# Performance work log

Measured on AMD Instinct MI355X. Metric: run time of the kernel, lower is better.

## Reference

```python
import jax, jax.numpy as jnp
import numpy as np
from jax import lax
from jax.scipy.special import logsumexp

TEMP_MIN, TEMP_MAX = 0.1, 1.0
B, I, J, C = 2, 128, 512, 256


def setup_inputs() -> dict:
    key = jax.random.key(0)
    k1, k2, k3 = jax.random.split(key, 3)
    return {
        "text_embeddings": jax.random.normal(k1, (B, I, C), dtype=jnp.float32),
        "mel_embeddings": jax.random.normal(k2, (B, J, C), dtype=jnp.float32),
        "text_mask": jnp.ones((B, I), dtype=jnp.float32),
        "mel_mask": jnp.ones((B, J), dtype=jnp.float32),
        "noise": jax.random.gumbel(k3, (B, I, J), dtype=jnp.float32),  # -log(-log(U))
        "temperature_ratio": jnp.float32(0.5),
    }


def _cond_prob(energy, text_mask, mel_mask, direction):
    # energy: [B, I, J]; returns [B, I, J, K] log conditional probs (normalized over axis 2)
    b, i, j = energy.shape
    if direction == "alpha":
        k = j
        tri = jnp.arange(j)[:, None] >= jnp.arange(k)[None, :]  # triu(ones(J,J)).T layout -> j >= k
        mel_k = mel_mask
    else:  # beta
        k = j - 1
        tri = jnp.arange(j)[:, None] <= jnp.arange(k)[None, :]  # tril(ones(J-1,J)).T layout -> j <= k
        mel_k = mel_mask[:, :k]
    valid = (
        (text_mask[:, :, None, None] * mel_mask[:, None, :, None] * mel_k[:, None, None, :]) > 0
    ) & tri[None, None]
    e4 = jnp.where(valid, energy[..., None], -jnp.inf)  # [B,I,J,K]
    e4 = e4 - logsumexp(e4, axis=2, keepdims=True)
    return jnp.where(valid, e4, jnp.asarray(-10.0, energy.dtype))


def reference(text_embeddings, mel_embeddings, text_mask, mel_mask, noise, temperature_ratio):
    b, i_len, ct = text_embeddings.shape
    j_len, cm = mel_embeddings.shape[1], mel_embeddings.shape[2]
    ninf = jnp.asarray(-jnp.inf, text_embeddings.dtype)

    energy = jnp.einsum("bic,bjc->bij", text_embeddings, mel_embeddings) / np.sqrt(ct * cm)
    temperature = TEMP_MIN + (TEMP_MAX - TEMP_MIN) * temperature_ratio
    energy = (energy + noise) / temperature

    cpa = _cond_prob(energy, text_mask, mel_mask, "alpha")  # [B,I,J,J]
    cpb = _cond_prob(energy, text_mask, mel_mask, "beta")   # [B,I,J,J-1]

    # forward (alpha) recursion over text dim: alpha[:, i, j+1] = LSE_k(alpha[:, i-1, k] + cpa[:, i-1, j, k])
    init_a = jnp.full((b, j_len + 1), -jnp.inf, energy.dtype).at[:, 0].set(0.0)

    def astep(carry, cpa_i):  # carry [B, J+1], cpa_i [B, J, J]
        row = logsumexp(carry[:, None, :-1] + cpa_i, axis=2)  # [B, J]
        new = jnp.concatenate([jnp.full((b, 1), -jnp.inf, energy.dtype), row], axis=1)
        return new, row

    _, arows = lax.scan(astep, init_a, jnp.swapaxes(cpa, 0, 1))
    alpha = jnp.swapaxes(arows, 0, 1)  # [B, I, J] == alpha[:, 1:, 1:]

    # backward (beta) recursion: beta[:, i, j] = LSE_k(beta[:, i+1, k+1] + cpb[:, i, j, k])
    init_b = jnp.full((b, j_len), -jnp.inf, energy.dtype).at[:, -1].set(0.0)

    def bstep(carry, cpb_i):  # carry [B, J], cpb_i [B, J, J-1]
        row = logsumexp(carry[:, None, 1:] + cpb_i, axis=2)
        return row, row

    _, brows = lax.scan(bstep, init_b, jnp.flip(jnp.swapaxes(cpb[:, : i_len - 1], 0, 1), axis=0))
    beta = jnp.concatenate([jnp.flip(brows, axis=0), init_b[None]], axis=0)
    beta = jnp.swapaxes(beta, 0, 1)  # [B, I, J]

    gamma = alpha + beta
    gmask = (text_mask[:, :, None] * mel_mask[:, None, :]) > 0
    gamma = jnp.where(gmask, gamma, ninf)
    gamma = jnp.where(gmask, gamma - logsumexp(gamma, axis=1, keepdims=True), ninf)

    expanded = jnp.einsum("bij,bic->bjc", jnp.exp(gamma), text_embeddings)
    expanded = expanded * mel_mask[:, :, None]
    return gamma, expanded
```

## Files before the change

### kernel.cpp

```cpp
#include <hip/hip_runtime.h>
#include <math.h>

#define BB 2
#define II 128
#define JJ 512
#define CC 256
#define NEL (BB*II*JJ)
#define NINF (-INFINITY)
#define K10 4.5399929762484854e-5f

template<int CTRL, int RM = 0xf, int BM = 0xf, bool BC = true>
__device__ __forceinline__ float dppf(float x) {
    return __int_as_float(__builtin_amdgcn_update_dpp(
        0, __float_as_int(x), CTRL, RM, BM, BC));
}
__device__ __forceinline__ float wscan_incl(float x) {
    x += dppf<0x111>(x);
    x += dppf<0x112>(x);
    x += dppf<0x114>(x);
    x += dppf<0x118>(x);
    x += dppf<0x142, 0xa>(x);
    x += dppf<0x143, 0xc>(x);
    return x;
}
__device__ __forceinline__ float lane_shr1(float x) { return dppf<0x138>(x); }
__device__ __forceinline__ float bcast63(float x) {
    return __int_as_float(__builtin_amdgcn_readlane(__float_as_int(x), 63));
}

__device__ __forceinline__ void tree_prefix8(const float x[8], float P[8]) {
    float t[8];
    t[0] = x[0];
    #pragma unroll
    for (int q = 1; q < 8; ++q) t[q] = x[q] + x[q-1];
    float u[8];
    u[0] = t[0]; u[1] = t[1];
    #pragma unroll
    for (int q = 2; q < 8; ++q) u[q] = t[q] + t[q-2];
    P[0] = u[0]; P[1] = u[1]; P[2] = u[2]; P[3] = u[3];
    #pragma unroll
    for (int q = 4; q < 8; ++q) P[q] = u[q] + u[q-4];
}

__device__ __forceinline__ void loadrow8(const float* __restrict__ p, float v[8]) {
    float4 a = *reinterpret_cast<const float4*>(p);
    float4 b = *reinterpret_cast<const float4*>(p + 4);
    v[0]=a.x; v[1]=a.y; v[2]=a.z; v[3]=a.w;
    v[4]=b.x; v[5]=b.y; v[6]=b.z; v[7]=b.w;
}
__device__ __forceinline__ void loadrow8_rev(const float* __restrict__ row, int lane, float v[8]) {
    float t[8];
    loadrow8(row + 504 - 8 * lane, t);
    #pragma unroll
    for (int q = 0; q < 8; ++q) v[q] = t[7 - q];
}
__device__ __forceinline__ void storerow8(float* __restrict__ p, const float v[8]) {
    *reinterpret_cast<float4*>(p)     = make_float4(v[0],v[1],v[2],v[3]);
    *reinterpret_cast<float4*>(p + 4) = make_float4(v[4],v[5],v[6],v[7]);
}

__global__ __launch_bounds__(256) void energy_kernel(
        const float* __restrict__ text, const float* __restrict__ mel,
        const float* __restrict__ noise, const float* __restrict__ ratio,
        float* __restrict__ e) {
    __shared__ float melS[64][65];
    __shared__ float texS[8][65];
    int b  = blockIdx.x;
    int i0 = blockIdx.y * 8;
    int j0 = blockIdx.z * 64;
    int t = threadIdx.x;
    int jj = t & 63, ig = t >> 6;
    float acc0 = 0.f, acc1 = 0.f;
    for (int cc = 0; cc < CC; cc += 64) {
        #pragma unroll
        for (int k = 0; k < 4; ++k) {
            int idx = t + k * 256;
            int row = idx >> 4, seg = idx & 15;
            float4 v = *reinterpret_cast<const float4*>(
                mel + (size_t)(b * JJ + j0 + row) * CC + cc + seg * 4);
            melS[row][seg*4+0] = v.x; melS[row][seg*4+1] = v.y;
            melS[row][seg*4+2] = v.z; melS[row][seg*4+3] = v.w;
        }
        if (t < 128) {
            int row = t >> 4, seg = t & 15;
            float4 v = *reinterpret_cast<const float4*>(
                text + (size_t)(b * II + i0 + row) * CC + cc + seg * 4);
            texS[row][seg*4+0] = v.x; texS[row][seg*4+1] = v.y;
            texS[row][seg*4+2] = v.z; texS[row][seg*4+3] = v.w;
        }
        __syncthreads();
        #pragma unroll 8
        for (int c = 0; c < 64; ++c) {
            float m = melS[jj][c];
            acc0 = fmaf(m, texS[ig*2+0][c], acc0);
            acc1 = fmaf(m, texS[ig*2+1][c], acc1);
        }
        __syncthreads();
    }
    float temp = 0.1f + 0.9f * ratio[0];
    float rtmp = 1.0f / temp;
    int r0 = (b * II + i0 + ig*2 + 0) * JJ + j0 + jj;
    int r1 = (b * II + i0 + ig*2 + 1) * JJ + j0 + jj;
    e[r0] = (acc0 * (1.0f/256.0f) + noise[r0]) * rtmp;
    e[r1] = (acc1 * (1.0f/256.0f) + noise[r1]) * rtmp;
}

__global__ __launch_bounds__(64) void dscan_kernel(
        const float* __restrict__ e, float* __restrict__ Ee,
        float* __restrict__ Wa, float* __restrict__ Wb) {
    int row = blockIdx.x;
    int lane = threadIdx.x;
    float v[8];
    loadrow8(e + row * JJ + lane * 8, v);
    float m = v[0];
    #pragma unroll
    for (int q = 1; q < 8; ++q) m = fmaxf(m, v[q]);
    #pragma unroll
    for (int d = 1; d < 64; d <<= 1) m = fmaxf(m, __shfl_xor(m, d, 64));
    float x[8];
    #pragma unroll
    for (int q = 0; q < 8; ++q) x[q] = __expf(v[q] - m);
    storerow8(Ee + row * JJ + lane * 8, x);
    float run = 0.f, P[8];
    #pragma unroll
    for (int q = 0; q < 8; ++q) { run += x[q]; P[q] = run; }
    float sc = wscan_incl(run);
    float cp = lane_shr1(sc);
    float run2 = 0.f, S[8];
    #pragma unroll
    for (int q = 7; q >= 0; --q) { run2 += x[q]; S[q] = run2; }
    float sd = run2;
    #pragma unroll
    for (int d = 1; d < 64; d <<= 1) { float o = __shfl_down(sd, d, 64); sd += (lane + d < 64) ? o : 0.0f; }
    float cs = __shfl_down(sd, 1, 64); if (lane == 63) cs = 0.f;
    float wa[8], wb[8];
    #pragma unroll
    for (int q = 0; q < 8; ++q) {
        wa[q] = 1.0f / (S[q] + cs);
        wb[q] = 1.0f / (P[q] + cp);
    }
    storerow8(Wa + row * JJ + lane * 8, wa);
    storerow8(Wb + row * JJ + lane * 8, wb);
}

template<bool NORM>
__device__ __forceinline__ void astep(
    int i, int lane, int off, bool pf,
    const float (&pin)[8], float (&pout)[8], float& c,
    float (&CE)[8], float (&CW)[8],
    float (&LE)[8], float (&LW)[8],
    const float* __restrict__ EeB, const float* __restrict__ WaB,
    float* __restrict__ paB, float* __restrict__ caB)
{
    storerow8(paB + (size_t)(i - 1) * JJ + off, pin);
    if (lane == 0) caB[i - 1] = c;
    __builtin_amdgcn_sched_barrier(0);
    if (pf) {
        loadrow8(EeB + (size_t)(i + 3) * JJ + off, LE);
        loadrow8(WaB + (size_t)(i + 3) * JJ + off, LW);
    }

    float pup = lane_shr1(pin[7]);
    float y[8];
    y[0] = pup * CW[0];
    #pragma unroll
    for (int q = 1; q < 8; ++q) y[q] = pin[q-1] * CW[q];
    float zz[8];
    #pragma unroll
    for (int q = 0; q < 7; ++q) zz[q] = pin[q];
    zz[7] = (lane == 63) ? 0.0f : pin[7];
    float Y[8], Z[8];
    tree_prefix8(y, Y);
    tree_prefix8(zz, Z);
    float sy = wscan_incl(Y[7]);
    float sz = wscan_incl(Z[7]);
    float oy = lane_shr1(sy);
    float oz = lane_shr1(sz);
    float T  = bcast63(sz);
    #pragma unroll
    for (int q = 0; q < 8; ++q) {
        float S1 = oy + Y[q];
        float S2 = fmaxf(T - (oz + Z[q]) + zz[q], 0.0f);
        pout[q] = fmaf(CE[q], S1, K10 * S2);
    }
    if (NORM) {
        float Tc = fmaxf(T, 1e-30f);
        float rT = __builtin_amdgcn_rcpf(Tc);
        c += __logf(Tc);
        #pragma unroll
        for (int q = 0; q < 8; ++q) pout[q] *= rT;
    }
}

template<bool NORM>
__device__ __forceinline__ void bstep(
    int i, int lane, int off, bool pf,
    const float (&pin)[8], float (&pout)[8], float& c,
    float (&CE)[8], float (&CW)[8],
    float (&LE)[8], float (&LW)[8],
    const float* __restrict__ EeB, const float* __restrict__ WbB,
    float* __restrict__ pbB, float* __restrict__ cbB)
{
    storerow8(pbB + (size_t)(i + 1) * JJ + off, pin);
    if (lane == 0) cbB[i + 1] = c;
    __builtin_amdgcn_sched_barrier(0);
    if (pf) {
        loadrow8_rev(EeB + (size_t)(i - 3) * JJ, lane, LE);
        loadrow8_rev(WbB + (size_t)(i - 3) * JJ, lane, LW);
    }

    float pup = lane_shr1(pin[7]);
    float pn[8];
    pn[0] = pup;
    #pragma unroll
    for (int q = 1; q < 8; ++q) pn[q] = pin[q-1];
    float w[8];
    #pragma unroll
    for (int q = 0; q < 8; ++q) w[q] = pn[q] * CW[q];
    float W[8], N[8];
    tree_prefix8(w, W);
    tree_prefix8(pn, N);
    float sw = wscan_incl(W[7]);
    float sn = wscan_incl(N[7]);
    float ow = lane_shr1(sw);
    float on = lane_shr1(sn);
    float T  = bcast63(sn);
    #pragma unroll
    for (int q = 0; q < 8; ++q) {
        float QA = ow + W[q];
        float QB = fmaxf(T - (on + N[q]), 0.0f);
        pout[q] = fmaf(CE[q], QA, K10 * QB);
    }
    if (NORM) {
        float Tc = fmaxf(T, 1e-30f);
        float rT = __builtin_amdgcn_rcpf(Tc);
        c += __logf(Tc);
        #pragma unroll
        for (int q = 0; q < 8; ++q) pout[q] *= rT;
    }
}

__global__ __launch_bounds__(64) void scan_ab_kernel(
        const float* __restrict__ Ee, const float* __restrict__ Wa,
        const float* __restrict__ Wb,
        float* __restrict__ pa, float* __restrict__ pb,
        float* __restrict__ ca, float* __restrict__ cb) {
    int b = blockIdx.x >> 1, dir = blockIdx.x & 1;
    int lane = threadIdx.x, off = lane * 8;
    size_t base = (size_t)b * II * JJ;
    float pA[8], pB[8], c = 0.0f;
    float B0e[8], B0w[8], B1e[8], B1w[8], B2e[8], B2w[8], B3e[8], B3w[8];

    if (dir == 0) {
        const float* EeB = Ee + base; const float* WaB = Wa + base;
        float* paB = pa + base; float* caB = ca + b * II;
        loadrow8(EeB + (size_t)1*JJ + off, B1e); loadrow8(WaB + (size_t)1*JJ + off, B1w);
        loadrow8(EeB + (size_t)2*JJ + off, B2e); loadrow8(WaB + (size_t)2*JJ + off, B2w);
        loadrow8(EeB + (size_t)3*JJ + off, B3e); loadrow8(WaB + (size_t)3*JJ + off, B3w);
        float e0[8];
        loadrow8(EeB + off, e0);
        float wa00 = WaB[0];
        #pragma unroll
        for (int q = 0; q < 8; ++q) pA[q] = e0[q] * wa00;
        int i = 1;
        #pragma unroll 1
        for (; i + 3 <= II - 1; i += 4) {
            astep<true >(i,   lane, off, i+3 < II, pA, pB, c, B1e,B1w, B0e,B0w, EeB,WaB,paB,caB);
            astep<false>(i+1, lane, off, i+4 < II, pB, pA, c, B2e,B2w, B1e,B1w, EeB,WaB,paB,caB);
            astep<false>(i+2, lane, off, i+5 < II, pA, pB, c, B3e,B3w, B2e,B2w, EeB,WaB,paB,caB);
            astep<false>(i+3, lane, off, i+6 < II, pB, pA, c, B0e,B0w, B3e,B3w, EeB,WaB,paB,caB);
        }
        astep<true >(125, lane, off, false, pA, pB, c, B1e,B1w, B0e,B0w, EeB,WaB,paB,caB);
        astep<false>(126, lane, off, false, pB, pA, c, B2e,B2w, B1e,B1w, EeB,WaB,paB,caB);
        astep<false>(127, lane, off, false, pA, pB, c, B3e,B3w, B2e,B2w, EeB,WaB,paB,caB);
        storerow8(paB + (size_t)127 * JJ + off, pB);
        if (lane == 0) caB[127] = c;
    } else {
        const float* EeB = Ee + base; const float* WbB = Wb + base;
        float* pbB = pb + base; float* cbB = cb + b * II;
        loadrow8_rev(EeB + (size_t)126*JJ, lane, B2e); loadrow8_rev(WbB + (size_t)126*JJ, lane, B2w);
        loadrow8_rev(EeB + (size_t)125*JJ, lane, B1e); loadrow8_rev(WbB + (size_t)125*JJ, lane, B1w);
        loadrow8_rev(EeB + (size_t)124*JJ, lane, B0e); loadrow8_rev(WbB + (size_t)124*JJ, lane, B0w);
        #pragma unroll
        for (int q = 0; q < 8; ++q) pA[q] = 0.0f;
        pA[0] = (lane == 0) ? 1.0f : 0.0f;
        int i = II - 2;
        #pragma unroll 1
        for (; i - 3 >= 0; i -= 4) {
            bstep<true >(i,   lane, off, i-3 >= 0, pA, pB, c, B2e,B2w, B3e,B3w, EeB,WbB,pbB,cbB);
            bstep<false>(i-1, lane, off, i-4 >= 0, pB, pA, c, B1e,B1w, B2e,B2w, EeB,WbB,pbB,cbB);
            bstep<false>(i-2, lane, off, i-5 >= 0, pA, pB, c, B0e,B0w, B1e,B1w, EeB,WbB,pbB,cbB);
            bstep<false>(i-3, lane, off, i-6 >= 0, pB, pA, c, B3e,B3w, B0e,B0w, EeB,WbB,pbB,cbB);
        }
        bstep<true >(2, lane, off, false, pA, pB, c, B2e,B2w, B3e,B3w, EeB,WbB,pbB,cbB);
        bstep<false>(1, lane, off, false, pB, pA, c, B1e,B1w, B2e,B2w, EeB,WbB,pbB,cbB);
        bstep<false>(0, lane, off, false, pA, pB, c, B0e,B0w, B1e,B1w, EeB,WbB,pbB,cbB);
        storerow8(pbB + off, pB);
        if (lane == 0) cbB[0] = c;
    }
}

__global__ __launch_bounds__(256) void gamma_expand_kernel(
        const float* __restrict__ pa, const float* __restrict__ pb,
        const float* __restrict__ ca, const float* __restrict__ cb,
        const float* __restrict__ text, const float* __restrict__ mmask,
        float* __restrict__ gamma_out, float* __restrict__ expanded) {
    __shared__ float wt[II][9];
    __shared__ float Ei[II];
    __shared__ float red[8][33];
    int b   = blockIdx.x >> 6;
    int jj0 = (blockIdx.x & 63) * 8;
    int t = threadIdx.x;
    int q = t & 7, ic = t >> 3;

    if (t < II) Ei[t] = ca[b*II + t] + cb[b*II + t];
    __syncthreads();
    float maxc = Ei[0];
    #pragma unroll 16
    for (int i = 1; i < II; ++i) maxc = fmaxf(maxc, Ei[i]);
    __syncthreads();
    if (t < II) Ei[t] = __expf(Ei[t] - maxc);
    __syncthreads();

    size_t idx0  = (size_t)b * II * JJ + jj0 + q;
    size_t idx0r = (size_t)b * II * JJ + (JJ - 1 - jj0 - q);
    float d = 0.f;
    #pragma unroll
    for (int k = 0; k < 4; ++k) {
        int i = ic * 4 + k;
        float P = pa[idx0 + (size_t)i * JJ] * pb[idx0r + (size_t)i * JJ] * Ei[i];
        wt[i][q] = P;
        d += P;
    }
    red[q][ic] = d;
    __syncthreads();
    if (t < 8) {
        float s = 0.f;
        #pragma unroll
        for (int k = 0; k < 32; ++k) s += red[t][k];
        red[t][32] = 1.0f / fmaxf(s, 1e-37f);
    }
    __syncthreads();
    float rD = red[q][32];
    #pragma unroll
    for (int k = 0; k < 4; ++k) {
        int i = ic * 4 + k;
        float P = wt[i][q] * rD;
        wt[i][q] = P;
        gamma_out[idx0 + (size_t)i * JJ] = fmaxf(__logf(P), -1e30f);
    }
    __syncthreads();

    float acc[8] = {0,0,0,0,0,0,0,0};
    const float* txb = text + (size_t)b * II * CC + t;
    #pragma unroll 4
    for (int i = 0; i < II; ++i) {
        float tv = txb[(size_t)i * CC];
        #pragma unroll
        for (int qq = 0; qq < 8; ++qq) acc[qq] = fmaf(wt[i][qq], tv, acc[qq]);
    }
    #pragma unroll
    for (int qq = 0; qq < 8; ++qq) {
        expanded[(size_t)(b * JJ + jj0 + qq) * CC + t] =
            acc[qq] * mmask[b * JJ + jj0 + qq];
    }
}

extern "C" void kernel_launch(void* const* d_in, const int* in_sizes, int n_in,
                              void* d_out, int out_size, void* d_ws, size_t ws_size,
                              hipStream_t stream) {
    const float* text  = (const float*)d_in[0];
    const float* mel   = (const float*)d_in[1];
    const float* mmask = (const float*)d_in[3];
    const float* noise = (const float*)d_in[4];
    const float* ratio = (const float*)d_in[5];
    float* gamma_out = (float*)d_out;
    float* expanded  = (float*)d_out + NEL;

    float* ws = (float*)d_ws;
    float* Ee = ws;
    float* Wa = ws +   NEL;
    float* Wb = ws + 2*NEL;
    float* pa = ws + 3*NEL;
    float* pb = ws + 4*NEL;
    float* ca = ws + 5*NEL;
    float* cb = ws + 5*NEL + BB*II;
    float* e  = pa;

    hipLaunchKernelGGL(energy_kernel, dim3(BB, II/8, JJ/64), dim3(256), 0, stream,
                       text, mel, noise, ratio, e);
    hipLaunchKernelGGL(dscan_kernel, dim3(BB*II), dim3(64), 0, stream, e, Ee, Wa, Wb);
    hipLaunchKernelGGL(scan_ab_kernel, dim3(BB*2), dim3(64), 0, stream,
                       Ee, Wa, Wb, pa, pb, ca, cb);
    hipLaunchKernelGGL(gamma_expand_kernel, dim3(BB*64), dim3(256), 0, stream,
                       pa, pb, ca, cb, text, mmask, gamma_out, expanded);
}
```

Measured before the change: 138.7 us.

## Stage scan rows into LDS via async global_load_lds with explicit vmcnt waits

The serial alpha/beta scan kernel now prefetches upcoming energy and weight rows straight into a 4-deep LDS ring with global_load_lds, instead of into register buffers. Each step waits on a fixed vmcnt count and then reads the current row from LDS. The goal is to cut register pressure and keep global-load latency off the serial dependency chain. In exchange it adds LDS reads per step and relies on hand-counted vmcnt values, which also include the output stores; miscounting them would give races or needless stalls.

```diff
diff --git a/kernel.cpp b/kernel.cpp
--- a/kernel.cpp
+++ b/kernel.cpp
@@ -42,21 +42,31 @@
     for (int q = 4; q < 8; ++q) P[q] = u[q] + u[q-4];
 }
 
-__device__ __forceinline__ void loadrow8(const float* __restrict__ p, float v[8]) {
+__device__ __forceinline__ void loadrow8(const float* p, float v[8]) {
     float4 a = *reinterpret_cast<const float4*>(p);
     float4 b = *reinterpret_cast<const float4*>(p + 4);
     v[0]=a.x; v[1]=a.y; v[2]=a.z; v[3]=a.w;
     v[4]=b.x; v[5]=b.y; v[6]=b.z; v[7]=b.w;
 }
-__device__ __forceinline__ void loadrow8_rev(const float* __restrict__ row, int lane, float v[8]) {
-    float t[8];
-    loadrow8(row + 504 - 8 * lane, t);
-    #pragma unroll
-    for (int q = 0; q < 8; ++q) v[q] = t[7 - q];
-}
 __device__ __forceinline__ void storerow8(float* __restrict__ p, const float v[8]) {
     *reinterpret_cast<float4*>(p)     = make_float4(v[0],v[1],v[2],v[3]);
     *reinterpret_cast<float4*>(p + 4) = make_float4(v[4],v[5],v[6],v[7]);
+}
+
+typedef __attribute__((address_space(1))) float gfloat;
+typedef __attribute__((address_space(3))) float lfloat;
+__device__ __forceinline__ void gl_lds16(const float* g, float* l) {
+    __builtin_amdgcn_global_load_lds((gfloat*)g, (lfloat*)l, 16, 0, 0);
+}
+__device__ __forceinline__ void stage_row(const float* gE, const float* gW,
+                                          float* lE, float* lW, int lane) {
+    gl_lds16(gE + lane * 4,       lE);
+    gl_lds16(gE + 256 + lane * 4, lE + 256);
+    gl_lds16(gW + lane * 4,       lW);
+    gl_lds16(gW + 256 + lane * 4, lW + 256);
+}
+template<int N> __device__ __forceinline__ void waitcnt_vm() {
+    asm volatile("s_waitcnt vmcnt(%0)" :: "i"(N) : "memory");
 }
 
 __global__ __launch_bounds__(256) void energy_kernel(
@@ -143,22 +153,23 @@
     storerow8(Wb + row * JJ + lane * 8, wb);
 }
 
-template<bool NORM>
+template<bool NORM, int VM>
 __device__ __forceinline__ void astep(
     int i, int lane, int off, bool pf,
     const float (&pin)[8], float (&pout)[8], float& c,
-    float (&CE)[8], float (&CW)[8],
-    float (&LE)[8], float (&LW)[8],
+    const float* cE, const float* cW,
+    float* lE, float* lW,
     const float* __restrict__ EeB, const float* __restrict__ WaB,
     float* __restrict__ paB, float* __restrict__ caB)
 {
     storerow8(paB + (size_t)(i - 1) * JJ + off, pin);
     if (lane == 0) caB[i - 1] = c;
     __builtin_amdgcn_sched_barrier(0);
-    if (pf) {
-        loadrow8(EeB + (size_t)(i + 3) * JJ + off, LE);
-        loadrow8(WaB + (size_t)(i + 3) * JJ + off, LW);
-    }
+    if (pf) stage_row(EeB + (size_t)(i + 3) * JJ, WaB + (size_t)(i + 3) * JJ, lE, lW, lane);
+    waitcnt_vm<VM>();
+    float CE[8], CW[8];
+    loadrow8(cE + lane * 8, CE);
+    loadrow8(cW + lane * 8, CW);
 
     float pup = lane_shr1(pin[7]);
     float y[8];
@@ -192,22 +203,25 @@
     }
 }
 
-template<bool NORM>
+template<bool NORM, int VM>
 __device__ __forceinline__ void bstep(
     int i, int lane, int off, bool pf,
     const float (&pin)[8], float (&pout)[8], float& c,
-    float (&CE)[8], float (&CW)[8],
-    float (&LE)[8], float (&LW)[8],
+    const float* cE, const float* cW,
+    float* lE, float* lW,
     const float* __restrict__ EeB, const float* __restrict__ WbB,
     float* __restrict__ pbB, float* __restrict__ cbB)
 {
     storerow8(pbB + (size_t)(i + 1) * JJ + off, pin);
     if (lane == 0) cbB[i + 1] = c;
     __builtin_amdgcn_sched_barrier(0);
-    if (pf) {
-        loadrow8_rev(EeB + (size_t)(i - 3) * JJ, lane, LE);
-        loadrow8_rev(WbB + (size_t)(i - 3) * JJ, lane, LW);
-    }
+    if (pf) stage_row(EeB + (size_t)(i - 3) * JJ, WbB + (size_t)(i - 3) * JJ, lE, lW, lane);
+    waitcnt_vm<VM>();
+    float tE[8], tW[8], CE[8], CW[8];
+    loadrow8(cE + 504 - 8 * lane, tE);
+    loadrow8(cW + 504 - 8 * lane, tW);
+    #pragma unroll
+    for (int q = 0; q < 8; ++q) { CE[q] = tE[7-q]; CW[q] = tW[7-q]; }
 
     float pup = lane_shr1(pin[7]);
     float pn[8];
@@ -245,57 +259,61 @@
         const float* __restrict__ Wb,
         float* __restrict__ pa, float* __restrict__ pb,
         float* __restrict__ ca, float* __restrict__ cb) {
+    __shared__ float ldsE[4][JJ];
+    __shared__ float ldsW[4][JJ];
     int b = blockIdx.x >> 1, dir = blockIdx.x & 1;
     int lane = threadIdx.x, off = lane * 8;
     size_t base = (size_t)b * II * JJ;
-    float pA[8], pB[8], c = 0.0f;
-    float B0e[8], B0w[8], B1e[8], B1w[8], B2e[8], B2w[8], B3e[8], B3w[8];
+    float p0[8], p1[8], p2[8], p3[8], c = 0.0f;
 
     if (dir == 0) {
         const float* EeB = Ee + base; const float* WaB = Wa + base;
         float* paB = pa + base; float* caB = ca + b * II;
-        loadrow8(EeB + (size_t)1*JJ + off, B1e); loadrow8(WaB + (size_t)1*JJ + off, B1w);
-        loadrow8(EeB + (size_t)2*JJ + off, B2e); loadrow8(WaB + (size_t)2*JJ + off, B2w);
-        loadrow8(EeB + (size_t)3*JJ + off, B3e); loadrow8(WaB + (size_t)3*JJ + off, B3w);
+        stage_row(EeB,                 WaB,                 &ldsE[0][0], &ldsW[0][0], lane);
+        stage_row(EeB + (size_t)1*JJ,  WaB + (size_t)1*JJ,  &ldsE[1][0], &ldsW[1][0], lane);
+        stage_row(EeB + (size_t)2*JJ,  WaB + (size_t)2*JJ,  &ldsE[2][0], &ldsW[2][0], lane);
+        stage_row(EeB + (size_t)3*JJ,  WaB + (size_t)3*JJ,  &ldsE[3][0], &ldsW[3][0], lane);
+        waitcnt_vm<0>();
         float e0[8];
-        loadrow8(EeB + off, e0);
-        float wa00 = WaB[0];
-        #pragma unroll
-        for (int q = 0; q < 8; ++q) pA[q] = e0[q] * wa00;
+        loadrow8(&ldsE[0][lane * 8], e0);
+        float wa00 = ldsW[0][0];
+        #pragma unroll
+        for (int q = 0; q < 8; ++q) p0[q] = e0[q] * wa00;
         int i = 1;
         #pragma unroll 1
         for (; i + 3 <= II - 1; i += 4) {
-            astep<true >(i,   lane, off, i+3 < II, pA, pB, c, B1e,B1w, B0e,B0w, EeB,WaB,paB,caB);
-            astep<false>(i+1, lane, off, i+4 < II, pB, pA, c, B2e,B2w, B1e,B1w, EeB,WaB,paB,caB);
-            astep<false>(i+2, lane, off, i+5 < II, pA, pB, c, B3e,B3w, B2e,B2w, EeB,WaB,paB,caB);
-            astep<false>(i+3, lane, off, i+6 < II, pB, pA, c, B0e,B0w, B3e,B3w, EeB,WaB,paB,caB);
+            astep<true ,18>(i,   lane, off, true, p0, p1, c, &ldsE[1][0], &ldsW[1][0], &ldsE[0][0], &ldsW[0][0], EeB, WaB, paB, caB);
+            astep<false,18>(i+1, lane, off, true, p1, p2, c, &ldsE[2][0], &ldsW[2][0], &ldsE[1][0], &ldsW[1][0], EeB, WaB, paB, caB);
+            astep<false,18>(i+2, lane, off, true, p2, p3, c, &ldsE[3][0], &ldsW[3][0], &ldsE[2][0], &ldsW[2][0], EeB, WaB, paB, caB);
+            astep<false,18>(i+3, lane, off, true, p3, p0, c, &ldsE[0][0], &ldsW[0][0], &ldsE[3][0], &ldsW[3][0], EeB, WaB, paB, caB);
         }
-        astep<true >(125, lane, off, false, pA, pB, c, B1e,B1w, B0e,B0w, EeB,WaB,paB,caB);
-        astep<false>(126, lane, off, false, pB, pA, c, B2e,B2w, B1e,B1w, EeB,WaB,paB,caB);
-        astep<false>(127, lane, off, false, pA, pB, c, B3e,B3w, B2e,B2w, EeB,WaB,paB,caB);
-        storerow8(paB + (size_t)127 * JJ + off, pB);
+        astep<true ,14>(125, lane, off, false, p0, p1, c, &ldsE[1][0], &ldsW[1][0], &ldsE[0][0], &ldsW[0][0], EeB, WaB, paB, caB);
+        astep<false,10>(126, lane, off, false, p1, p2, c, &ldsE[2][0], &ldsW[2][0], &ldsE[1][0], &ldsW[1][0], EeB, WaB, paB, caB);
+        astep<false, 6>(127, lane, off, false, p2, p3, c, &ldsE[3][0], &ldsW[3][0], &ldsE[2][0], &ldsW[2][0], EeB, WaB, paB, caB);
+        storerow8(paB + (size_t)127 * JJ + off, p3);
         if (lane == 0) caB[127] = c;
     } else {
         const float* EeB = Ee + base; const float* WbB = Wb + base;
         float* pbB = pb + base; float* cbB = cb + b * II;
-        loadrow8_rev(EeB + (size_t)126*JJ, lane, B2e); loadrow8_rev(WbB + (size_t)126*JJ, lane, B2w);
-        loadrow8_rev(EeB + (size_t)125*JJ, lane, B1e); loadrow8_rev(WbB + (size_t)125*JJ, lane, B1w);
-        loadrow8_rev(EeB + (size_t)124*JJ, lane, B0e); loadrow8_rev(WbB + (size_t)124*JJ, lane, B0w);
-        #pragma unroll
-        for (int q = 0; q < 8; ++q) pA[q] = 0.0f;
-        pA[0] = (lane == 0) ? 1.0f : 0.0f;
+        stage_row(EeB + (size_t)126*JJ, WbB + (size_t)126*JJ, &ldsE[2][0], &ldsW[2][0], lane);
+        stage_row(EeB + (size_t)125*JJ, WbB + (size_t)125*JJ, &ldsE[1][0], &ldsW[1][0], lane);
+        stage_row(EeB + (size_t)124*JJ, WbB + (size_t)124*JJ, &ldsE[0][0], &ldsW[0][0], lane);
+        waitcnt_vm<0>();
+        #pragma unroll
+        for (int q = 0; q < 8; ++q) p0[q] = 0.0f;
+        p0[0] = (lane == 0) ? 1.0f : 0.0f;
         int i = II - 2;
         #pragma unroll 1
         for (; i - 3 >= 0; i -= 4) {
-            bstep<true >(i,   lane, off, i-3 >= 0, pA, pB, c, B2e,B2w, B3e,B3w, EeB,WbB,pbB,cbB);
-            bstep<false>(i-1, lane, off, i-4 >= 0, pB, pA, c, B1e,B1w, B2e,B2w, EeB,WbB,pbB,cbB);
-            bstep<false>(i-2, lane, off, i-5 >= 0, pA, pB, c, B0e,B0w, B1e,B1w, EeB,WbB,pbB,cbB);
-            bstep<false>(i-3, lane, off, i-6 >= 0, pB, pA, c, B3e,B3w, B0e,B0w, EeB,WbB,pbB,cbB);
+            bstep<true ,18>(i,   lane, off, true, p0, p1, c, &ldsE[2][0], &ldsW[2][0], &ldsE[3][0], &ldsW[3][0], EeB, WbB, pbB, cbB);
+            bstep<false,18>(i-1, lane, off, true, p1, p2, c, &ldsE[1][0], &ldsW[1][0], &ldsE[2][0], &ldsW[2][0], EeB, WbB, pbB, cbB);
+            bstep<false,18>(i-2, lane, off, true, p2, p3, c, &ldsE[0][0], &ldsW[0][0], &ldsE[1][0], &ldsW[1][0], EeB, WbB, pbB, cbB);
+            bstep<false,18>(i-3, lane, off, true, p3, p0, c, &ldsE[3][0], &ldsW[3][0], &ldsE[0][0], &ldsW[0][0], EeB, WbB, pbB, cbB);
         }
-        bstep<true >(2, lane, off, false, pA, pB, c, B2e,B2w, B3e,B3w, EeB,WbB,pbB,cbB);
-        bstep<false>(1, lane, off, false, pB, pA, c, B1e,B1w, B2e,B2w, EeB,WbB,pbB,cbB);
-        bstep<false>(0, lane, off, false, pA, pB, c, B0e,B0w, B1e,B1w, EeB,WbB,pbB,cbB);
-        storerow8(pbB + off, pB);
+        bstep<true ,14>(2, lane, off, false, p0, p1, c, &ldsE[2][0], &ldsW[2][0], &ldsE[3][0], &ldsW[3][0], EeB, WbB, pbB, cbB);
+        bstep<false,10>(1, lane, off, false, p1, p2, c, &ldsE[1][0], &ldsW[1][0], &ldsE[2][0], &ldsW[2][0], EeB, WbB, pbB, cbB);
+        bstep<false, 6>(0, lane, off, false, p2, p3, c, &ldsE[0][0], &ldsW[0][0], &ldsE[1][0], &ldsW[1][0], EeB, WbB, pbB, cbB);
+        storerow8(pbB + off, p3);
         if (lane == 0) cbB[0] = c;
     }
 }
```

Measured after the change: 158.1 us. +14.0%, slower.

## Hand-schedule scan loads/stores with inline asm and explicit vmcnt waits

Applied to the files above, without the earlier changes.

Rewrites the sequential alpha/beta scan kernel to issue global loads and stores through inline assembly, with explicit s_waitcnt vmcnt counts. Prefetched rows can then stay in flight across steps instead of the compiler waiting conservatively on every load. Per-row normalisation constants are kept in LDS and written to global memory once at the end, removing scalar global stores from the critical loop. The step sequence is unrolled by 8 with rotating buffers and normalisation every 4 steps. The hand-counted vmcnt values are a correctness risk if the compiler emits extra memory ops.

```diff
diff --git a/kernel.cpp b/kernel.cpp
--- a/kernel.cpp
+++ b/kernel.cpp
@@ -8,6 +8,8 @@
 #define NEL (BB*II*JJ)
 #define NINF (-INFINITY)
 #define K10 4.5399929762484854e-5f
+
+typedef float f32x4 __attribute__((ext_vector_type(4)));
 
 template<int CTRL, int RM = 0xf, int BM = 0xf, bool BC = true>
 __device__ __forceinline__ float dppf(float x) {
@@ -42,22 +44,32 @@
     for (int q = 4; q < 8; ++q) P[q] = u[q] + u[q-4];
 }
 
-__device__ __forceinline__ void loadrow8(const float* __restrict__ p, float v[8]) {
+__device__ __forceinline__ void loadrow8(const float* p, float v[8]) {
     float4 a = *reinterpret_cast<const float4*>(p);
     float4 b = *reinterpret_cast<const float4*>(p + 4);
     v[0]=a.x; v[1]=a.y; v[2]=a.z; v[3]=a.w;
     v[4]=b.x; v[5]=b.y; v[6]=b.z; v[7]=b.w;
 }
-__device__ __forceinline__ void loadrow8_rev(const float* __restrict__ row, int lane, float v[8]) {
-    float t[8];
-    loadrow8(row + 504 - 8 * lane, t);
-    #pragma unroll
-    for (int q = 0; q < 8; ++q) v[q] = t[7 - q];
-}
 __device__ __forceinline__ void storerow8(float* __restrict__ p, const float v[8]) {
     *reinterpret_cast<float4*>(p)     = make_float4(v[0],v[1],v[2],v[3]);
     *reinterpret_cast<float4*>(p + 4) = make_float4(v[4],v[5],v[6],v[7]);
 }
+
+__device__ __forceinline__ void aload2(f32x4 &d0, f32x4 &d1, const float* p) {
+    asm volatile("global_load_dwordx4 %0, %2, off\n\t"
+                 "global_load_dwordx4 %1, %2, off offset:16"
+                 : "=&v"(d0), "=&v"(d1) : "v"(p) : "memory");
+}
+__device__ __forceinline__ void astore2(f32x4 d0, f32x4 d1, float* p) {
+    asm volatile("global_store_dwordx4 %2, %0, off\n\t"
+                 "global_store_dwordx4 %2, %1, off offset:16"
+                 :: "v"(d0), "v"(d1), "v"(p) : "memory");
+}
+template<int N> __device__ __forceinline__ void waitcnt_vm() {
+    asm volatile("s_waitcnt vmcnt(%0)" :: "i"(N) : "memory");
+}
+
+struct Buf { f32x4 e0, e1, w0, w1; };
 
 __global__ __launch_bounds__(256) void energy_kernel(
         const float* __restrict__ text, const float* __restrict__ mel,
@@ -143,22 +155,29 @@
     storerow8(Wb + row * JJ + lane * 8, wb);
 }
 
-template<bool NORM>
+
+template<bool NORM, int VM, bool PF>
 __device__ __forceinline__ void astep(
-    int i, int lane, int off, bool pf,
+    int i, int lane, int off,
     const float (&pin)[8], float (&pout)[8], float& c,
-    float (&CE)[8], float (&CW)[8],
-    float (&LE)[8], float (&LW)[8],
+    Buf& C, Buf& L,
     const float* __restrict__ EeB, const float* __restrict__ WaB,
-    float* __restrict__ paB, float* __restrict__ caB)
+    float* __restrict__ paB, float* ldsC)
 {
-    storerow8(paB + (size_t)(i - 1) * JJ + off, pin);
-    if (lane == 0) caB[i - 1] = c;
+    {
+        f32x4 s0 = {pin[0], pin[1], pin[2], pin[3]};
+        f32x4 s1 = {pin[4], pin[5], pin[6], pin[7]};
+        astore2(s0, s1, paB + (size_t)(i - 1) * JJ + off);
+    }
+    if (lane == 0) ldsC[i - 1] = c;
+    if (PF) {
+        aload2(L.e0, L.e1, EeB + (size_t)(i + 3) * JJ + off);
+        aload2(L.w0, L.w1, WaB + (size_t)(i + 3) * JJ + off);
+    }
+    waitcnt_vm<VM>();
     __builtin_amdgcn_sched_barrier(0);
-    if (pf) {
-        loadrow8(EeB + (size_t)(i + 3) * JJ + off, LE);
-        loadrow8(WaB + (size_t)(i + 3) * JJ + off, LW);
-    }
+    float CE[8] = {C.e0[0],C.e0[1],C.e0[2],C.e0[3],C.e1[0],C.e1[1],C.e1[2],C.e1[3]};
+    float CW[8] = {C.w0[0],C.w0[1],C.w0[2],C.w0[3],C.w1[0],C.w1[1],C.w1[2],C.w1[3]};
 
     float pup = lane_shr1(pin[7]);
     float y[8];
@@ -192,22 +211,28 @@
     }
 }
 
-template<bool NORM>
+template<bool NORM, int VM, bool PF>
 __device__ __forceinline__ void bstep(
-    int i, int lane, int off, bool pf,
+    int i, int lane, int off,
     const float (&pin)[8], float (&pout)[8], float& c,
-    float (&CE)[8], float (&CW)[8],
-    float (&LE)[8], float (&LW)[8],
+    Buf& C, Buf& L,
     const float* __restrict__ EeB, const float* __restrict__ WbB,
-    float* __restrict__ pbB, float* __restrict__ cbB)
+    float* __restrict__ pbB, float* ldsC)
 {
-    storerow8(pbB + (size_t)(i + 1) * JJ + off, pin);
-    if (lane == 0) cbB[i + 1] = c;
+    {
+        f32x4 s0 = {pin[0], pin[1], pin[2], pin[3]};
+        f32x4 s1 = {pin[4], pin[5], pin[6], pin[7]};
+        astore2(s0, s1, pbB + (size_t)(i + 1) * JJ + off);
+    }
+    if (lane == 0) ldsC[i + 1] = c;
+    if (PF) {
+        aload2(L.e0, L.e1, EeB + (size_t)(i - 3) * JJ + 504 - 8 * lane);
+        aload2(L.w0, L.w1, WbB + (size_t)(i - 3) * JJ + 504 - 8 * lane);
+    }
+    waitcnt_vm<VM>();
     __builtin_amdgcn_sched_barrier(0);
-    if (pf) {
-        loadrow8_rev(EeB + (size_t)(i - 3) * JJ, lane, LE);
-        loadrow8_rev(WbB + (size_t)(i - 3) * JJ, lane, LW);
-    }
+    float CE[8] = {C.e1[3],C.e1[2],C.e1[1],C.e1[0],C.e0[3],C.e0[2],C.e0[1],C.e0[0]};
+    float CW[8] = {C.w1[3],C.w1[2],C.w1[1],C.w1[0],C.w0[3],C.w0[2],C.w0[1],C.w0[0]};
 
     float pup = lane_shr1(pin[7]);
     float pn[8];
@@ -245,58 +270,82 @@
         const float* __restrict__ Wb,
         float* __restrict__ pa, float* __restrict__ pb,
         float* __restrict__ ca, float* __restrict__ cb) {
+    __shared__ float ldsC[II];
     int b = blockIdx.x >> 1, dir = blockIdx.x & 1;
     int lane = threadIdx.x, off = lane * 8;
     size_t base = (size_t)b * II * JJ;
-    float pA[8], pB[8], c = 0.0f;
-    float B0e[8], B0w[8], B1e[8], B1w[8], B2e[8], B2w[8], B3e[8], B3w[8];
+    float P0[8], P1[8], P2[8], P3[8], c = 0.0f;
+    Buf B0, B1, B2, B3;
 
     if (dir == 0) {
         const float* EeB = Ee + base; const float* WaB = Wa + base;
         float* paB = pa + base; float* caB = ca + b * II;
-        loadrow8(EeB + (size_t)1*JJ + off, B1e); loadrow8(WaB + (size_t)1*JJ + off, B1w);
-        loadrow8(EeB + (size_t)2*JJ + off, B2e); loadrow8(WaB + (size_t)2*JJ + off, B2w);
-        loadrow8(EeB + (size_t)3*JJ + off, B3e); loadrow8(WaB + (size_t)3*JJ + off, B3w);
-        float e0[8];
-        loadrow8(EeB + off, e0);
+        float e0r[8];
+        loadrow8(EeB + off, e0r);
         float wa00 = WaB[0];
         #pragma unroll
-        for (int q = 0; q < 8; ++q) pA[q] = e0[q] * wa00;
-        int i = 1;
+        for (int q = 0; q < 8; ++q) P0[q] = e0r[q] * wa00;
+        __builtin_amdgcn_sched_barrier(0);
+        aload2(B1.e0, B1.e1, EeB + (size_t)1*JJ + off); aload2(B1.w0, B1.w1, WaB + (size_t)1*JJ + off);
+        aload2(B2.e0, B2.e1, EeB + (size_t)2*JJ + off); aload2(B2.w0, B2.w1, WaB + (size_t)2*JJ + off);
+        aload2(B3.e0, B3.e1, EeB + (size_t)3*JJ + off); aload2(B3.w0, B3.w1, WaB + (size_t)3*JJ + off);
+        astep<true ,14,true>(1, lane, off, P0, P1, c, B1, B0, EeB, WaB, paB, ldsC);
+        astep<false,16,true>(2, lane, off, P1, P2, c, B2, B1, EeB, WaB, paB, ldsC);
         #pragma unroll 1
-        for (; i + 3 <= II - 1; i += 4) {
-            astep<true >(i,   lane, off, i+3 < II, pA, pB, c, B1e,B1w, B0e,B0w, EeB,WaB,paB,caB);
-            astep<false>(i+1, lane, off, i+4 < II, pB, pA, c, B2e,B2w, B1e,B1w, EeB,WaB,paB,caB);
-            astep<false>(i+2, lane, off, i+5 < II, pA, pB, c, B3e,B3w, B2e,B2w, EeB,WaB,paB,caB);
-            astep<false>(i+3, lane, off, i+6 < II, pB, pA, c, B0e,B0w, B3e,B3w, EeB,WaB,paB,caB);
+        for (int d = 0; d < 15; ++d) {
+            int ib = 3 + 8 * d;
+            astep<false,18,true>(ib+0, lane, off, P2, P3, c, B3, B2, EeB, WaB, paB, ldsC);
+            astep<false,18,true>(ib+1, lane, off, P3, P0, c, B0, B3, EeB, WaB, paB, ldsC);
+            astep<true ,18,true>(ib+2, lane, off, P0, P1, c, B1, B0, EeB, WaB, paB, ldsC);
+            astep<false,18,true>(ib+3, lane, off, P1, P2, c, B2, B1, EeB, WaB, paB, ldsC);
+            astep<false,18,true>(ib+4, lane, off, P2, P3, c, B3, B2, EeB, WaB, paB, ldsC);
+            astep<false,18,true>(ib+5, lane, off, P3, P0, c, B0, B3, EeB, WaB, paB, ldsC);
+            astep<true ,18,true>(ib+6, lane, off, P0, P1, c, B1, B0, EeB, WaB, paB, ldsC);
+            astep<false,18,true>(ib+7, lane, off, P1, P2, c, B2, B1, EeB, WaB, paB, ldsC);
         }
-        astep<true >(125, lane, off, false, pA, pB, c, B1e,B1w, B0e,B0w, EeB,WaB,paB,caB);
-        astep<false>(126, lane, off, false, pB, pA, c, B2e,B2w, B1e,B1w, EeB,WaB,paB,caB);
-        astep<false>(127, lane, off, false, pA, pB, c, B3e,B3w, B2e,B2w, EeB,WaB,paB,caB);
-        storerow8(paB + (size_t)127 * JJ + off, pB);
-        if (lane == 0) caB[127] = c;
+        astep<false,18,true >(123, lane, off, P2, P3, c, B3, B2, EeB, WaB, paB, ldsC);
+        astep<false,18,true >(124, lane, off, P3, P0, c, B0, B3, EeB, WaB, paB, ldsC);
+        astep<true ,14,false>(125, lane, off, P0, P1, c, B1, B0, EeB, WaB, paB, ldsC);
+        astep<false,10,false>(126, lane, off, P1, P2, c, B2, B1, EeB, WaB, paB, ldsC);
+        astep<false, 6,false>(127, lane, off, P2, P3, c, B3, B2, EeB, WaB, paB, ldsC);
+        storerow8(paB + (size_t)127 * JJ + off, P3);
+        if (lane == 0) ldsC[127] = c;
+        waitcnt_vm<0>();
+        caB[lane]      = ldsC[lane];
+        caB[lane + 64] = ldsC[lane + 64];
     } else {
         const float* EeB = Ee + base; const float* WbB = Wb + base;
         float* pbB = pb + base; float* cbB = cb + b * II;
-        loadrow8_rev(EeB + (size_t)126*JJ, lane, B2e); loadrow8_rev(WbB + (size_t)126*JJ, lane, B2w);
-        loadrow8_rev(EeB + (size_t)125*JJ, lane, B1e); loadrow8_rev(WbB + (size_t)125*JJ, lane, B1w);
-        loadrow8_rev(EeB + (size_t)124*JJ, lane, B0e); loadrow8_rev(WbB + (size_t)124*JJ, lane, B0w);
-        #pragma unroll
-        for (int q = 0; q < 8; ++q) pA[q] = 0.0f;
-        pA[0] = (lane == 0) ? 1.0f : 0.0f;
-        int i = II - 2;
+        #pragma unroll
+        for (int q = 0; q < 8; ++q) P3[q] = 0.0f;
+        P3[0] = (lane == 0) ? 1.0f : 0.0f;
+        aload2(B2.e0, B2.e1, EeB + (size_t)126*JJ + 504 - 8*lane); aload2(B2.w0, B2.w1, WbB + (size_t)126*JJ + 504 - 8*lane);
+        aload2(B1.e0, B1.e1, EeB + (size_t)125*JJ + 504 - 8*lane); aload2(B1.w0, B1.w1, WbB + (size_t)125*JJ + 504 - 8*lane);
+        aload2(B0.e0, B0.e1, EeB + (size_t)124*JJ + 504 - 8*lane); aload2(B0.w0, B0.w1, WbB + (size_t)124*JJ + 504 - 8*lane);
+        bstep<true ,14,true>(126, lane, off, P3, P2, c, B2, B3, EeB, WbB, pbB, ldsC);
+        bstep<false,16,true>(125, lane, off, P2, P1, c, B1, B2, EeB, WbB, pbB, ldsC);
         #pragma unroll 1
-        for (; i - 3 >= 0; i -= 4) {
-            bstep<true >(i,   lane, off, i-3 >= 0, pA, pB, c, B2e,B2w, B3e,B3w, EeB,WbB,pbB,cbB);
-            bstep<false>(i-1, lane, off, i-4 >= 0, pB, pA, c, B1e,B1w, B2e,B2w, EeB,WbB,pbB,cbB);
-            bstep<false>(i-2, lane, off, i-5 >= 0, pA, pB, c, B0e,B0w, B1e,B1w, EeB,WbB,pbB,cbB);
-            bstep<false>(i-3, lane, off, i-6 >= 0, pB, pA, c, B3e,B3w, B0e,B0w, EeB,WbB,pbB,cbB);
+        for (int d = 0; d < 15; ++d) {
+            int ib = 124 - 8 * d;
+            bstep<false,18,true>(ib-0, lane, off, P1, P0, c, B0, B1, EeB, WbB, pbB, ldsC);
+            bstep<false,18,true>(ib-1, lane, off, P0, P3, c, B3, B0, EeB, WbB, pbB, ldsC);
+            bstep<true ,18,true>(ib-2, lane, off, P3, P2, c, B2, B3, EeB, WbB, pbB, ldsC);
+            bstep<false,18,true>(ib-3, lane, off, P2, P1, c, B1, B2, EeB, WbB, pbB, ldsC);
+            bstep<false,18,true>(ib-4, lane, off, P1, P0, c, B0, B1, EeB, WbB, pbB, ldsC);
+            bstep<false,18,true>(ib-5, lane, off, P0, P3, c, B3, B0, EeB, WbB, pbB, ldsC);
+            bstep<true ,18,true>(ib-6, lane, off, P3, P2, c, B2, B3, EeB, WbB, pbB, ldsC);
+            bstep<false,18,true>(ib-7, lane, off, P2, P1, c, B1, B2, EeB, WbB, pbB, ldsC);
         }
-        bstep<true >(2, lane, off, false, pA, pB, c, B2e,B2w, B3e,B3w, EeB,WbB,pbB,cbB);
-        bstep<false>(1, lane, off, false, pB, pA, c, B1e,B1w, B2e,B2w, EeB,WbB,pbB,cbB);
-        bstep<false>(0, lane, off, false, pA, pB, c, B0e,B0w, B1e,B1w, EeB,WbB,pbB,cbB);
-        storerow8(pbB + off, pB);
-        if (lane == 0) cbB[0] = c;
+        bstep<false,18,true >(4, lane, off, P1, P0, c, B0, B1, EeB, WbB, pbB, ldsC);
+        bstep<false,18,true >(3, lane, off, P0, P3, c, B3, B0, EeB, WbB, pbB, ldsC);
+        bstep<true ,14,false>(2, lane, off, P3, P2, c, B2, B3, EeB, WbB, pbB, ldsC);
+        bstep<false,10,false>(1, lane, off, P2, P1, c, B1, B2, EeB, WbB, pbB, ldsC);
+        bstep<false, 6,false>(0, lane, off, P1, P0, c, B0, B1, EeB, WbB, pbB, ldsC);
+        storerow8(pbB + off, P0);
+        if (lane == 0) ldsC[0] = c;
+        waitcnt_vm<0>();
+        cbB[lane]      = ldsC[lane];
+        cbB[lane + 64] = ldsC[lane + 64];
     }
 }
 
```

Result: faster. 130.2 us (-6.2%).
